# Performance work log

Hardware: AMD Instinct MI355X
Metric: run time of the kernel (lower is better)

Reference implementation:

```python
import jax, jax.numpy as jnp
import numpy as np

CUTOFF = 5.0
NUM_RADIAL = 6
HIDDEN = 128
N_NODES = 100000
N_EDGES = 800000
MAX_Z = 95
P = 6  # envelope_exponent(5) + 1, per PyG Envelope


def _envelope(x):
    # PyG DimeNet Envelope: (1/x + a*x^(p-1) + b*x^p + c*x^(p+1)) * (x < 1)
    a = -(P + 1) * (P + 2) / 2.0   # -28
    b = P * (P + 2)                # 48
    c = -P * (P + 1) / 2.0         # -21
    xp0 = x ** (P - 1)
    xp1 = xp0 * x
    xp2 = xp1 * x
    return (1.0 / x + a * xp0 + b * xp1 + c * xp2) * (x < 1.0)


def setup_inputs():
    key = jax.random.key(0)
    ks = jax.random.split(key, 8)
    z = jax.random.randint(ks[0], (N_NODES,), 0, MAX_Z, dtype=jnp.int32)
    pos = jax.random.normal(ks[1], (N_NODES, 3), dtype=jnp.float32)
    ei = jax.random.randint(ks[2], (2, N_EDGES), 0, N_NODES, dtype=jnp.int32)
    i, j = ei[0], ei[1]
    j = jnp.where(j == i, (j + 1) % N_NODES, j)  # radius_graph emits no self-loops (avoids d=0)
    edge_index = jnp.stack([i, j])
    # BesselBasisLayer learnable frequencies: pi * n
    freq = np.pi * jnp.arange(1, NUM_RADIAL + 1, dtype=jnp.float32)
    s3 = float(np.sqrt(3.0))
    emb_table = jax.random.uniform(ks[3], (MAX_Z, HIDDEN), jnp.float32, -s3, s3)
    W_rbf = jax.random.normal(ks[4], (NUM_RADIAL, HIDDEN), jnp.float32) * (1.0 / np.sqrt(NUM_RADIAL))
    b_rbf = jnp.zeros((HIDDEN,), jnp.float32)
    W_lin = jax.random.normal(ks[5], (3 * HIDDEN, HIDDEN), jnp.float32) * (1.0 / np.sqrt(3 * HIDDEN))
    b_lin = jnp.zeros((HIDDEN,), jnp.float32)
    return {"z": z, "pos": pos, "edge_index": edge_index, "freq": freq,
            "emb_table": emb_table, "W_rbf": W_rbf, "b_rbf": b_rbf,
            "W_lin": W_lin, "b_lin": b_lin}


def reference(z, pos, edge_index, freq, emb_table, W_rbf, b_rbf, W_lin, b_lin):
    n = z.shape[0]
    i, j = edge_index[0], edge_index[1]
    # per-edge distance  [E]
    d = jnp.sqrt(jnp.sum((pos[i] - pos[j]) ** 2, axis=-1))
    # Bessel RBF  [E, num_radial]
    x = d[:, None] / CUTOFF
    rbf = _envelope(x) * jnp.sin(freq * x)
    # DimeNet EmbeddingBlock (act = SiLU/swish)
    h_rbf = jax.nn.silu(rbf @ W_rbf + b_rbf)            # [E, H]
    xz = emb_table[z]                                    # [N, H]
    e_emb = jax.nn.silu(
        jnp.concatenate([xz[i], xz[j], h_rbf], axis=-1) @ W_lin + b_lin
    )                                                    # [E, H]
    # scatter_mean over target node j -> [N, H]
    sums = jax.ops.segment_sum(e_emb, j, num_segments=n)
    cnt = jax.ops.segment_sum(jnp.ones_like(d), j, num_segments=n)
    v_emb = sums / jnp.maximum(cnt, 1.0)[:, None]
    return v_emb  # pool=None -> node-level embeddings
```

## Files before the change

### kernel.cpp

```cpp
#include <hip/hip_runtime.h>
#include <hip/hip_bf16.h>
#include <math.h>

#define HID 128
#define NRAD 6
#define TABN 4096
#define CUTOFF_INV 0.2f
#define MZ 95
#define MZP (MZ + 1)
#define SENT ((MZ << 13) | (MZ << 20))
#define PAD 32
#define OVF_CAP 65536
#define FTR 8
#define LOG2E 1.4426950408889634f
#define LN2   0.6931471805599453f

typedef unsigned int uint32;

__global__ void build1(const float* __restrict__ emb, const float* __restrict__ W_lin,
                       const float* __restrict__ freq, const float* __restrict__ W_rbf,
                       const float* __restrict__ b_rbf, const float* __restrict__ b_lin,
                       const int* __restrict__ ei, const float* __restrict__ pos,
                       const int* __restrict__ z,
                       __hip_bfloat16* __restrict__ Tb, float* __restrict__ ftab,
                       int* __restrict__ cnt, int* __restrict__ payload,
                       int* __restrict__ ovfcnt, int2* __restrict__ ovfbuf,
                       int MAXZ, int E) {
    __shared__ float sh[FTR * HID];
    int h   = threadIdx.x;
    int bid = blockIdx.x;
    int nT  = 2 * (MAXZ + 1);
    int nF  = (TABN + FTR) / FTR;
    if (bid < nT) {
        int zz = bid >> 1, s = bid & 1;
        if (zz == MAXZ) {
            Tb[(size_t)(s * (MAXZ + 1) + zz) * HID + h] = __float2bfloat16(-86.5f);
            return;
        }
        sh[h] = emb[zz * HID + h];
        __syncthreads();
        const float* W = W_lin + (size_t)s * HID * HID;
        float acc = (s == 0) ? b_lin[h] : 0.f;
#pragma unroll 8
        for (int k = 0; k < HID; ++k) acc = fmaf(sh[k], W[k * HID + h], acc);
        Tb[(size_t)(s * (MAXZ + 1) + zz) * HID + h] = __float2bfloat16(acc * LOG2E);
    } else if (bid < nT + nF) {
        int t0 = (bid - nT) * FTR;
        for (int r = 0; r < FTR; ++r) {
            int t = t0 + r;
            float rbf[NRAD];
            if (t == 0) {
#pragma unroll
                for (int k = 0; k < NRAD; ++k) rbf[k] = freq[k];
            } else if (t >= TABN) {
#pragma unroll
                for (int k = 0; k < NRAD; ++k) rbf[k] = 0.f;
            } else {
                float x  = (float)t / (float)TABN;
                float x2 = x * x, x5 = x2 * x2 * x;
                float env = 1.f / x + x5 * (-28.f + x * (48.f + x * (-21.f)));
#pragma unroll
                for (int k = 0; k < NRAD; ++k) rbf[k] = env * sinf(freq[k] * x);
            }
            float pre = b_rbf[h];
#pragma unroll
            for (int k = 0; k < NRAD; ++k) pre = fmaf(rbf[k], W_rbf[k * HID + h], pre);
            sh[r * HID + h] = pre / (1.f + __expf(-pre));
        }
        __syncthreads();
        const float* W3 = W_lin + (size_t)2 * HID * HID;
        float acc[FTR];
#pragma unroll
        for (int r = 0; r < FTR; ++r) acc[r] = 0.f;
#pragma unroll 4
        for (int k = 0; k < HID; ++k) {
            float w = W3[k * HID + h];
#pragma unroll
            for (int r = 0; r < FTR; ++r) acc[r] = fmaf(sh[r * HID + k], w, acc[r]);
        }
        for (int r = 0; r < FTR; ++r) {
            int t = t0 + r;
            if (t <= TABN) ftab[(size_t)t * HID + h] = acc[r] * LOG2E;
        }
    } else {
        int e = (bid - nT - nF) * HID + h;
        if (e < E) {
            int i = ei[e];
            int j = ei[E + e];
            float dx = pos[3 * i]     - pos[3 * j];
            float dy = pos[3 * i + 1] - pos[3 * j + 1];
            float dz = pos[3 * i + 2] - pos[3 * j + 2];
            float d  = sqrtf(dx * dx + dy * dy + dz * dz);
            float u  = fminf(d * CUTOFF_INV, 1.0f) * (float)TABN;
            int   ti = (int)(u + 0.5f);
            if (ti > TABN) ti = TABN;
            int pl = ti | (z[i] << 13) | (z[j] << 20);
            int r  = atomicAdd(&cnt[j], 1);
            if (r < PAD) {
                payload[(size_t)j * PAD + r] = pl;
            } else {
                int o = atomicAdd(ovfcnt, 1);
                if (o < OVF_CAP) ovfbuf[o] = make_int2(j, pl);
            }
        }
    }
}

__device__ __forceinline__ float exp2neg(float x) {
    float r; asm("v_exp_f32 %0, -%1" : "=v"(r) : "v"(x)); return r;
}

#define PLSEL(pv_, idx_) (hi ? __builtin_amdgcn_readlane((pv_), 2 * (idx_) + 1) \
                             : __builtin_amdgcn_readlane((pv_), 2 * (idx_)))

#define FLOAD(pl_) (*(const float4*)((const char*)ftab + (uint32)((((pl_) & 0x1FFF) << 9) + fb4)))

#define TL(pl_, ua_, ub_) do {                                                 \
    int zi_ = ((pl_) >> 13) & 0x7F;                                            \
    int zj_ = ((pl_) >> 20) & 0x7F;                                            \
    ua_ = *(const uint2*)&sT[zi_ * (HID / 2) + l2];                            \
    ub_ = *(const uint2*)&sT[(MZP + zj_) * (HID / 2) + l2];                    \
} while (0)

#define COMPUTE(f_, ua_, ub_) do {                                                                 \
    float p0_ = __uint_as_float(ua_.x << 16)         + __uint_as_float(ub_.x << 16)         + f_.x; \
    float p1_ = __uint_as_float(ua_.x & 0xFFFF0000u) + __uint_as_float(ub_.x & 0xFFFF0000u) + f_.y; \
    float p2_ = __uint_as_float(ua_.y << 16)         + __uint_as_float(ub_.y << 16)         + f_.z; \
    float p3_ = __uint_as_float(ua_.y & 0xFFFF0000u) + __uint_as_float(ub_.y & 0xFFFF0000u) + f_.w; \
    ax = fmaf(p0_, __builtin_amdgcn_rcpf(1.f + exp2neg(p0_)), ax);                                 \
    ay = fmaf(p1_, __builtin_amdgcn_rcpf(1.f + exp2neg(p1_)), ay);                                 \
    az = fmaf(p2_, __builtin_amdgcn_rcpf(1.f + exp2neg(p2_)), az);                                 \
    aw = fmaf(p3_, __builtin_amdgcn_rcpf(1.f + exp2neg(p3_)), aw);                                 \
} while (0)

__launch_bounds__(1024)
__global__ void gather_k(const int* __restrict__ cnt, const int* __restrict__ payload,
                         const uint32* __restrict__ Tb32, const float* __restrict__ ftab,
                         const int* __restrict__ ovfcnt, const int2* __restrict__ ovfbuf,
                         float* __restrict__ out, int N) {
    __shared__ uint32 sT[2 * MZP * (HID / 2)];
    int tid = threadIdx.x;
    for (int k = tid; k < 2 * MZP * (HID / 2); k += 1024) sT[k] = Tb32[k];
    __syncthreads();

    int lane = tid & 63, wv = tid >> 6;
    int hi   = lane >> 5;
    int l32  = lane & 31;
    int h4   = l32 * 4;
    int l2   = l32 * 2;
    uint32 fb4 = (uint32)l32 << 4;
    int nov  = *ovfcnt;
    if (nov > OVF_CAP) nov = OVF_CAP;
    int nW = gridDim.x << 4;

    int n = (blockIdx.x << 4) + wv;
    int degC = 0, plvC = SENT;
    if (n < N) { degC = cnt[n]; plvC = payload[(size_t)n * PAD + l32]; }

    while (n < N) {
        int n2 = n + nW;
        int degN = 0, plvN = SENT;
        if (n2 < N) { degN = cnt[n2]; plvN = payload[(size_t)n2 * PAD + l32]; }

        int deg = degC;
        int cb  = deg < PAD ? deg : PAD;
        int plv = (l32 < cb) ? plvC : SENT;
        int nit = (cb + 1) >> 1;

        float ax = 0.f, ay = 0.f, az = 0.f, aw = 0.f;
        if (nit > 0) {
            int pl0 = PLSEL(plv, 0);
            float4 f0 = FLOAD(pl0);
            uint2 ua, ub; TL(pl0, ua, ub);
            int plL = PLSEL(plv, 1);
            float4 f1 = FLOAD(plL);
#pragma unroll 2
            for (int k = 0; k < nit; ++k) {
                int kk  = (k + 2) & 15;
                int pl2 = PLSEL(plv, kk);
                float4 f2 = FLOAD(pl2);
                uint2 va, vb; TL(plL, va, vb);
                COMPUTE(f0, ua, ub);
                f0 = f1; f1 = f2;
                ua = va; ub = vb;
                plL = pl2;
            }
        }
        if (deg > PAD && nov > 0) {
            for (int o = 0; o < nov; ++o) {
                int2 v = ovfbuf[o];
                if (v.x == n) {
                    int pl = v.y;
                    float4 f_ = FLOAD(pl);
                    uint2 ua_, ub_; TL(pl, ua_, ub_);
                    COMPUTE(f_, ua_, ub_);
                }
            }
        }
        ax += __shfl_xor(ax, 32);
        ay += __shfl_xor(ay, 32);
        az += __shfl_xor(az, 32);
        aw += __shfl_xor(aw, 32);
        if (hi == 0) {
            float s = (deg > 0) ? LN2 / (float)deg : 0.0f;
            float4 o4;
            o4.x = ax * s; o4.y = ay * s; o4.z = az * s; o4.w = aw * s;
            *(float4*)(out + (size_t)n * HID + h4) = o4;
        }
        n = n2; degC = degN; plvC = plvN;
    }
}

extern "C" void kernel_launch(void* const* d_in, const int* in_sizes, int n_in,
                              void* d_out, int out_size, void* d_ws, size_t ws_size,
                              hipStream_t stream) {
    const int*   z     = (const int*)d_in[0];
    const float* pos   = (const float*)d_in[1];
    const int*   ei    = (const int*)d_in[2];
    const float* freq  = (const float*)d_in[3];
    const float* emb   = (const float*)d_in[4];
    const float* W_rbf = (const float*)d_in[5];
    const float* b_rbf = (const float*)d_in[6];
    const float* W_lin = (const float*)d_in[7];
    const float* b_lin = (const float*)d_in[8];

    int N    = in_sizes[0];
    int E    = in_sizes[2] / 2;
    int MAXZ = in_sizes[4] / HID;
    float* out = (float*)d_out;

    int N_pad = ((N + 1024) / 1024) * 1024;

    char* ws = (char*)d_ws;
    size_t off = 0;
    auto alloc = [&](size_t bytes) { char* p = ws + off; off = (off + bytes + 255) & ~(size_t)255; return p; };
    int*   cnt     = (int*)alloc((size_t)N_pad * 4);
    int*   ovfcnt  = (int*)alloc(256);
    __hip_bfloat16* Tb = (__hip_bfloat16*)alloc((size_t)2 * (MAXZ + 1) * HID * 2);
    float* ftab    = (float*)alloc((size_t)(TABN + 1) * HID * 4);
    int*   payload = (int*)alloc((size_t)N_pad * PAD * 4);
    int2*  ovfbuf  = (int2*)alloc((size_t)OVF_CAP * 8);

    hipMemsetAsync(cnt, 0, (size_t)N_pad * 4 + 256, stream);

    int nBuild = 2 * (MAXZ + 1) + (TABN + FTR) / FTR + (E + HID - 1) / HID;
    build1<<<nBuild, HID, 0, stream>>>(emb, W_lin, freq, W_rbf, b_rbf, b_lin,
                                       ei, pos, z, Tb, ftab, cnt, payload,
                                       ovfcnt, ovfbuf, MAXZ, E);
    gather_k<<<512, 1024, 0, stream>>>(cnt, payload, (const uint32*)Tb, ftab,
                                       ovfcnt, ovfbuf, out, N);
}
```

Measured before the change: 188.3 us.

## Pack node position and atomic number into float4 and split edge pass into own kernel

```diff
diff --git a/kernel.cpp b/kernel.cpp
--- a/kernel.cpp
+++ b/kernel.cpp
@@ -17,15 +17,13 @@
 
 typedef unsigned int uint32;
 
-__global__ void build1(const float* __restrict__ emb, const float* __restrict__ W_lin,
-                       const float* __restrict__ freq, const float* __restrict__ W_rbf,
-                       const float* __restrict__ b_rbf, const float* __restrict__ b_lin,
-                       const int* __restrict__ ei, const float* __restrict__ pos,
-                       const int* __restrict__ z,
-                       __hip_bfloat16* __restrict__ Tb, float* __restrict__ ftab,
-                       int* __restrict__ cnt, int* __restrict__ payload,
-                       int* __restrict__ ovfcnt, int2* __restrict__ ovfbuf,
-                       int MAXZ, int E) {
+__global__ void tabs_pack_k(const float* __restrict__ emb, const float* __restrict__ W_lin,
+                            const float* __restrict__ freq, const float* __restrict__ W_rbf,
+                            const float* __restrict__ b_rbf, const float* __restrict__ b_lin,
+                            const float* __restrict__ pos, const int* __restrict__ z,
+                            __hip_bfloat16* __restrict__ Tb, float* __restrict__ ftab,
+                            float4* __restrict__ pos4,
+                            int MAXZ, int N) {
     __shared__ float sh[FTR * HID];
     int h   = threadIdx.x;
     int bid = blockIdx.x;
@@ -83,26 +81,39 @@
             if (t <= TABN) ftab[(size_t)t * HID + h] = acc[r] * LOG2E;
         }
     } else {
-        int e = (bid - nT - nF) * HID + h;
-        if (e < E) {
-            int i = ei[e];
-            int j = ei[E + e];
-            float dx = pos[3 * i]     - pos[3 * j];
-            float dy = pos[3 * i + 1] - pos[3 * j + 1];
-            float dz = pos[3 * i + 2] - pos[3 * j + 2];
-            float d  = sqrtf(dx * dx + dy * dy + dz * dz);
-            float u  = fminf(d * CUTOFF_INV, 1.0f) * (float)TABN;
-            int   ti = (int)(u + 0.5f);
-            if (ti > TABN) ti = TABN;
-            int pl = ti | (z[i] << 13) | (z[j] << 20);
-            int r  = atomicAdd(&cnt[j], 1);
-            if (r < PAD) {
-                payload[(size_t)j * PAD + r] = pl;
-            } else {
-                int o = atomicAdd(ovfcnt, 1);
-                if (o < OVF_CAP) ovfbuf[o] = make_int2(j, pl);
-            }
-        }
+        int n = (bid - nT - nF) * HID + h;
+        if (n < N) {
+            float4 p;
+            p.x = pos[3 * n];
+            p.y = pos[3 * n + 1];
+            p.z = pos[3 * n + 2];
+            p.w = __int_as_float(z[n]);
+            pos4[n] = p;
+        }
+    }
+}
+
+__global__ void edge_k(const int* __restrict__ ei, const float4* __restrict__ pos4,
+                       int* __restrict__ cnt, int* __restrict__ payload,
+                       int* __restrict__ ovfcnt, int2* __restrict__ ovfbuf, int E) {
+    int e = blockIdx.x * 256 + threadIdx.x;
+    if (e >= E) return;
+    int i = ei[e];
+    int j = ei[E + e];
+    float4 pi = pos4[i];
+    float4 pj = pos4[j];
+    float dx = pi.x - pj.x, dy = pi.y - pj.y, dz = pi.z - pj.z;
+    float d  = sqrtf(dx * dx + dy * dy + dz * dz);
+    float u  = fminf(d * CUTOFF_INV, 1.0f) * (float)TABN;
+    int   ti = (int)(u + 0.5f);
+    if (ti > TABN) ti = TABN;
+    int pl = ti | (__float_as_int(pi.w) << 13) | (__float_as_int(pj.w) << 20);
+    int r  = atomicAdd(&cnt[j], 1);
+    if (r < PAD) {
+        payload[(size_t)j * PAD + r] = pl;
+    } else {
+        int o = atomicAdd(ovfcnt, 1);
+        if (o < OVF_CAP) ovfbuf[o] = make_int2(j, pl);
     }
 }
 
@@ -176,8 +187,7 @@
             float4 f1 = FLOAD(plL);
 #pragma unroll 2
             for (int k = 0; k < nit; ++k) {
-                int kk  = (k + 2) & 15;
-                int pl2 = PLSEL(plv, kk);
+                int pl2 = PLSEL(plv, k + 2);
                 float4 f2 = FLOAD(pl2);
                 uint2 va, vb; TL(plL, va, vb);
                 COMPUTE(f0, ua, ub);
@@ -240,13 +250,14 @@
     float* ftab    = (float*)alloc((size_t)(TABN + 1) * HID * 4);
     int*   payload = (int*)alloc((size_t)N_pad * PAD * 4);
     int2*  ovfbuf  = (int2*)alloc((size_t)OVF_CAP * 8);
+    float4* pos4   = (float4*)alloc((size_t)N_pad * 16);
 
     hipMemsetAsync(cnt, 0, (size_t)N_pad * 4 + 256, stream);
 
-    int nBuild = 2 * (MAXZ + 1) + (TABN + FTR) / FTR + (E + HID - 1) / HID;
-    build1<<<nBuild, HID, 0, stream>>>(emb, W_lin, freq, W_rbf, b_rbf, b_lin,
-                                       ei, pos, z, Tb, ftab, cnt, payload,
-                                       ovfcnt, ovfbuf, MAXZ, E);
+    int nTabs = 2 * (MAXZ + 1) + (TABN + FTR) / FTR + (N + HID - 1) / HID;
+    tabs_pack_k<<<nTabs, HID, 0, stream>>>(emb, W_lin, freq, W_rbf, b_rbf, b_lin,
+                                           pos, z, Tb, ftab, pos4, MAXZ, N);
+    edge_k<<<(E + 255) / 256, 256, 0, stream>>>(ei, pos4, cnt, payload, ovfcnt, ovfbuf, E);
     gather_k<<<512, 1024, 0, stream>>>(cnt, payload, (const uint32*)Tb, ftab,
                                        ovfcnt, ovfbuf, out, N);
 }
```

Result: slower. 201.2 us (+6.9%).

## Remap gather lanes to two channels per lane with packed f32 math

Applied to the files above, without the earlier changes.

```diff
diff --git a/kernel.cpp b/kernel.cpp
--- a/kernel.cpp
+++ b/kernel.cpp
@@ -16,6 +16,7 @@
 #define LN2   0.6931471805599453f
 
 typedef unsigned int uint32;
+typedef __attribute__((ext_vector_type(2))) float f2;
 
 __global__ void build1(const float* __restrict__ emb, const float* __restrict__ W_lin,
                        const float* __restrict__ freq, const float* __restrict__ W_rbf,
@@ -110,27 +111,23 @@
     float r; asm("v_exp_f32 %0, -%1" : "=v"(r) : "v"(x)); return r;
 }
 
-#define PLSEL(pv_, idx_) (hi ? __builtin_amdgcn_readlane((pv_), 2 * (idx_) + 1) \
-                             : __builtin_amdgcn_readlane((pv_), 2 * (idx_)))
-
-#define FLOAD(pl_) (*(const float4*)((const char*)ftab + (uint32)((((pl_) & 0x1FFF) << 9) + fb4)))
-
-#define TL(pl_, ua_, ub_) do {                                                 \
-    int zi_ = ((pl_) >> 13) & 0x7F;                                            \
-    int zj_ = ((pl_) >> 20) & 0x7F;                                            \
-    ua_ = *(const uint2*)&sT[zi_ * (HID / 2) + l2];                            \
-    ub_ = *(const uint2*)&sT[(MZP + zj_) * (HID / 2) + l2];                    \
-} while (0)
-
-#define COMPUTE(f_, ua_, ub_) do {                                                                 \
-    float p0_ = __uint_as_float(ua_.x << 16)         + __uint_as_float(ub_.x << 16)         + f_.x; \
-    float p1_ = __uint_as_float(ua_.x & 0xFFFF0000u) + __uint_as_float(ub_.x & 0xFFFF0000u) + f_.y; \
-    float p2_ = __uint_as_float(ua_.y << 16)         + __uint_as_float(ub_.y << 16)         + f_.z; \
-    float p3_ = __uint_as_float(ua_.y & 0xFFFF0000u) + __uint_as_float(ub_.y & 0xFFFF0000u) + f_.w; \
-    ax = fmaf(p0_, __builtin_amdgcn_rcpf(1.f + exp2neg(p0_)), ax);                                 \
-    ay = fmaf(p1_, __builtin_amdgcn_rcpf(1.f + exp2neg(p1_)), ay);                                 \
-    az = fmaf(p2_, __builtin_amdgcn_rcpf(1.f + exp2neg(p2_)), az);                                 \
-    aw = fmaf(p3_, __builtin_amdgcn_rcpf(1.f + exp2neg(p3_)), aw);                                 \
+#define FLOAD(pl_) (*(const f2*)((const char*)ftab + (uint32)((((pl_) & 0x1FFF) << 9) + fbyte)))
+
+#define TLA(pl_) sT[((((pl_) >> 13) & 0x7F) << 6) + lane]
+#define TLB(pl_) sT[sB + ((((pl_) >> 20) & 0x7F) << 6) + lane]
+
+#define COMPUTE(f_, ua_, ub_) do {                                             \
+    f2 A_, B_, P_, E_, R_;                                                     \
+    A_.x = __uint_as_float((ua_) << 16);                                       \
+    A_.y = __uint_as_float((ua_) & 0xFFFF0000u);                               \
+    B_.x = __uint_as_float((ub_) << 16);                                       \
+    B_.y = __uint_as_float((ub_) & 0xFFFF0000u);                               \
+    P_ = (A_ + B_) + f_;                                  \
+    E_.x = exp2neg(P_.x);  E_.y = exp2neg(P_.y);                               \
+    E_ = E_ + onev;                                              \
+    R_.x = __builtin_amdgcn_rcpf(E_.x);                                        \
+    R_.y = __builtin_amdgcn_rcpf(E_.y);                                        \
+    acc = __builtin_elementwise_fma(P_, R_, acc);            \
 } while (0)
 
 __launch_bounds__(1024)
@@ -143,70 +140,68 @@
     for (int k = tid; k < 2 * MZP * (HID / 2); k += 1024) sT[k] = Tb32[k];
     __syncthreads();
 
-    int lane = tid & 63, wv = tid >> 6;
-    int hi   = lane >> 5;
+    const int sB = MZP * (HID / 2);
+    int lane = tid & 63;
     int l32  = lane & 31;
-    int h4   = l32 * 4;
-    int l2   = l32 * 2;
-    uint32 fb4 = (uint32)l32 << 4;
-    int nov  = *ovfcnt;
+    int wv   = __builtin_amdgcn_readfirstlane(tid >> 6);
+    uint32 fbyte = (uint32)lane << 3;
+    f2 onev; onev.x = 1.f; onev.y = 1.f;
+    int nov  = __builtin_amdgcn_readfirstlane(*ovfcnt);
     if (nov > OVF_CAP) nov = OVF_CAP;
     int nW = gridDim.x << 4;
 
     int n = (blockIdx.x << 4) + wv;
     int degC = 0, plvC = SENT;
-    if (n < N) { degC = cnt[n]; plvC = payload[(size_t)n * PAD + l32]; }
+    if (n < N) {
+        degC = __builtin_amdgcn_readfirstlane(cnt[n]);
+        plvC = payload[(size_t)n * PAD + l32];
+    }
 
     while (n < N) {
         int n2 = n + nW;
         int degN = 0, plvN = SENT;
-        if (n2 < N) { degN = cnt[n2]; plvN = payload[(size_t)n2 * PAD + l32]; }
+        if (n2 < N) {
+            degN = __builtin_amdgcn_readfirstlane(cnt[n2]);
+            plvN = payload[(size_t)n2 * PAD + l32];
+        }
 
         int deg = degC;
         int cb  = deg < PAD ? deg : PAD;
         int plv = (l32 < cb) ? plvC : SENT;
-        int nit = (cb + 1) >> 1;
-
-        float ax = 0.f, ay = 0.f, az = 0.f, aw = 0.f;
-        if (nit > 0) {
-            int pl0 = PLSEL(plv, 0);
-            float4 f0 = FLOAD(pl0);
-            uint2 ua, ub; TL(pl0, ua, ub);
-            int plL = PLSEL(plv, 1);
-            float4 f1 = FLOAD(plL);
+
+        f2 acc; acc.x = 0.f; acc.y = 0.f;
+        if (cb > 0) {
+            int pl0 = __builtin_amdgcn_readlane(plv, 0);
+            f2 f0 = FLOAD(pl0);
+            uint32 ua = TLA(pl0), ub = TLB(pl0);
+            int plL = __builtin_amdgcn_readlane(plv, 1);
+            f2 f1 = FLOAD(plL);
 #pragma unroll 2
-            for (int k = 0; k < nit; ++k) {
-                int kk  = (k + 2) & 15;
-                int pl2 = PLSEL(plv, kk);
-                float4 f2 = FLOAD(pl2);
-                uint2 va, vb; TL(plL, va, vb);
+            for (int k = 0; k < cb; ++k) {
+                int pln = __builtin_amdgcn_readlane(plv, k + 2);
+                f2 fn = FLOAD(pln);
+                uint32 va = TLA(plL), vb = TLB(plL);
                 COMPUTE(f0, ua, ub);
-                f0 = f1; f1 = f2;
+                f0 = f1; f1 = fn;
                 ua = va; ub = vb;
-                plL = pl2;
+                plL = pln;
             }
         }
         if (deg > PAD && nov > 0) {
             for (int o = 0; o < nov; ++o) {
                 int2 v = ovfbuf[o];
-                if (v.x == n) {
-                    int pl = v.y;
-                    float4 f_ = FLOAD(pl);
-                    uint2 ua_, ub_; TL(pl, ua_, ub_);
+                int jn = __builtin_amdgcn_readfirstlane(v.x);
+                if (jn == n) {
+                    int pl = __builtin_amdgcn_readfirstlane(v.y);
+                    f2 f_ = FLOAD(pl);
+                    uint32 ua_ = TLA(pl), ub_ = TLB(pl);
                     COMPUTE(f_, ua_, ub_);
                 }
             }
         }
-        ax += __shfl_xor(ax, 32);
-        ay += __shfl_xor(ay, 32);
-        az += __shfl_xor(az, 32);
-        aw += __shfl_xor(aw, 32);
-        if (hi == 0) {
-            float s = (deg > 0) ? LN2 / (float)deg : 0.0f;
-            float4 o4;
-            o4.x = ax * s; o4.y = ay * s; o4.z = az * s; o4.w = aw * s;
-            *(float4*)(out + (size_t)n * HID + h4) = o4;
-        }
+        float s = (deg > 0) ? LN2 / (float)deg : 0.0f;
+        f2 o2; o2.x = acc.x * s; o2.y = acc.y * s;
+        *(f2*)(out + (size_t)n * HID + (lane << 1)) = o2;
         n = n2; degC = degN; plvC = plvN;
     }
 }
```

Measured after the change: 180.2 us. -4.3%, faster.
